# Kernel tuning notes

Hardware: AMD Instinct MI355X
Metric: run time of the kernel (lower is better)

## Reference

```python
import jax, jax.numpy as jnp
import numpy as np

B, T, C, H = 8, 2048, 768, 64

def setup_inputs() -> dict:
    key = jax.random.key(0)
    k1, k2, k3, k4 = jax.random.split(key, 4)
    x = jax.random.normal(k1, (B, T, C), dtype=jnp.float32)
    Wk = jax.random.normal(k2, (C, H), dtype=jnp.float32) * 0.02
    Wq = jax.random.normal(k3, (C, H), dtype=jnp.float32) * 0.02
    Wv = jax.random.normal(k4, (C, H), dtype=jnp.float32) * 0.02
    return {"x": x, "Wk": Wk, "Wq": Wq, "Wv": Wv}

def reference(x, Wk, Wq, Wv):
    # QKV projections (no bias): [B,T,C] @ [C,H] -> [B,T,H]
    k = jnp.einsum('btc,ch->bth', x, Wk)
    q = jnp.einsum('btc,ch->bth', x, Wq)
    v = jnp.einsum('btc,ch->bth', x, Wv)
    scale = 1.0 / jnp.sqrt(jnp.asarray(q.shape[-1], q.dtype))
    # scores: [B,T,T]
    wei = jnp.einsum('bth,bsh->bts', q, k) * scale
    # causal mask: upper triangle (k=1) set to -inf before softmax
    causal = jnp.tril(jnp.ones((wei.shape[1], wei.shape[2]), dtype=bool))
    wei = jnp.where(causal[None, :, :], wei, -jnp.inf)
    wei = jax.nn.softmax(wei, axis=-1)
    # dropout deterministic (training=False) -> identity
    out = jnp.einsum('bts,bsh->bth', wei, v)
    return out
```

## Files before the change

### kernel.cpp

```cpp
#include <hip/hip_runtime.h>
#include <hip/hip_bf16.h>
#include <stdint.h>

#define BB 8
#define TT 2048
#define CC 768
#define NTPB 72

typedef __bf16 bf16x8 __attribute__((ext_vector_type(8)));
typedef float f32x4 __attribute__((ext_vector_type(4)));
typedef float f32x16 __attribute__((ext_vector_type(16)));

__device__ inline __bf16 f2b(float f) {
    __hip_bfloat16 h = __float2bfloat16(f);
    return __builtin_bit_cast(__bf16, h);
}
__device__ inline ushort f2bits(float f) {
    __hip_bfloat16 h = __float2bfloat16(f);
    return __builtin_bit_cast(ushort, h);
}
__device__ inline float bits2f(ushort u) {
    return __builtin_bit_cast(float, ((uint32_t)u) << 16);
}
__device__ inline uint32_t cvtpk(float lo, float hi) {
    uint32_t r;
    asm("v_cvt_pk_bf16_f32 %0, %1, %2" : "=v"(r) : "v"(lo), "v"(hi));
    return r;
}
__device__ inline void pswap(uint32_t& a, uint32_t& b) {
    asm volatile("v_permlane32_swap_b32 %0, %1" : "+v"(a), "+v"(b));
}

#define GLL16(gp, lp)                                                          \
    __builtin_amdgcn_global_load_lds(                                          \
        (const __attribute__((address_space(1))) unsigned int*)(gp),           \
        (__attribute__((address_space(3))) unsigned int*)(lp), 16, 0, 0)

__launch_bounds__(256)
__global__ void wt_kernel(const float* __restrict__ Wk, const float* __restrict__ Wq,
                          const float* __restrict__ Wv, ushort* __restrict__ WtF) {
    __shared__ float tile[32][65];
    int m  = blockIdx.x / 24;
    int c0 = (blockIdx.x % 24) * 32;
    const float* W = (m == 0) ? Wq : ((m == 1) ? Wk : Wv);
    int tid = threadIdx.x;
    {
        int r   = tid >> 3;
        int col = (tid & 7) * 8;
        float4 v0 = *(const float4*)&W[(size_t)(c0 + r) * 64 + col];
        float4 v1 = *(const float4*)&W[(size_t)(c0 + r) * 64 + col + 4];
        tile[r][col]     = v0.x; tile[r][col + 1] = v0.y;
        tile[r][col + 2] = v0.z; tile[r][col + 3] = v0.w;
        tile[r][col + 4] = v1.x; tile[r][col + 5] = v1.y;
        tile[r][col + 6] = v1.z; tile[r][col + 7] = v1.w;
    }
    __syncthreads();
    int j   = tid >> 2;
    int sub = tid & 3;
    int cc  = sub * 8;
    ushort tmp[8];
#pragma unroll
    for (int e = 0; e < 8; e++) tmp[e] = f2bits(tile[cc + e][j]);
    int kc = c0 >> 5;
    ushort* dst = &WtF[((size_t)kc * 192 + m * 64 + j) * 32 + sub * 8];
    *(uint4*)(dst) = *(uint4*)&tmp[0];
}

__launch_bounds__(256, 3)
__global__ void qkv_kernel(const float* __restrict__ x, const ushort* __restrict__ WtF,
                           ushort* __restrict__ qws, ushort* __restrict__ kws,
                           ushort* __restrict__ vws) {
    __shared__ float  xsA[4][32 * 32];
    __shared__ ushort xsB[3][6144];

    int tid  = threadIdx.x;
    int wid  = tid >> 6;
    int lane = tid & 63;
    int l15  = lane & 15;
    int hi4  = lane >> 4;
    int row0 = blockIdx.x * 32;

    int rA  = tid >> 3;
    int gcA = (tid & 7) ^ (rA & 7);
    const float* gpA = x + (size_t)(row0 + rA) * CC + gcA * 4;

    int PB0 = tid, PB1 = tid + 256, PB2 = tid + 512;
    int LB0 = PB0 ^ ((PB0 >> 3) & 3);
    int LB1 = PB1 ^ ((PB1 >> 3) & 3);
    int LB2 = PB2 ^ ((PB2 >> 3) & 3);

    int PrB[3];
#pragma unroll
    for (int nt = 0; nt < 3; nt++) {
        int Lr = (wid * 48 + nt * 16 + l15) * 4 + hi4;
        PrB[nt] = Lr ^ ((Lr >> 3) & 3);
    }

    f32x4 acc[2][3];
#pragma unroll
    for (int mm = 0; mm < 2; mm++)
#pragma unroll
        for (int nt = 0; nt < 3; nt++) acc[mm][nt] = (f32x4){0.f, 0.f, 0.f, 0.f};

    auto stageA = [&](int t) {
        GLL16(gpA + t * 32, &xsA[t & 3][(size_t)tid * 4]);
    };
    auto stageB = [&](int t) {
        int buf = t % 3;
        const ushort* bsrc = WtF + (size_t)t * 6144;
        GLL16(bsrc + LB0 * 8, &xsB[buf][PB0 * 8]);
        GLL16(bsrc + LB1 * 8, &xsB[buf][PB1 * 8]);
        GLL16(bsrc + LB2 * 8, &xsB[buf][PB2 * 8]);
    };

    stageA(0); stageA(1);
    stageB(0); stageB(1);
    stageA(2); stageA(3);

#pragma unroll
    for (int p = 0; p < 12; p++) {
        if (p < 11) asm volatile("s_waitcnt vmcnt(2)" ::: "memory");
        else        asm volatile("s_waitcnt vmcnt(0)" ::: "memory");
        __builtin_amdgcn_s_barrier();
        __builtin_amdgcn_sched_barrier(0);

#pragma unroll
        for (int u = 0; u < 2; u++) {
            int t    = 2 * p + u;
            int bufA = t & 3;
            int bufB = t % 3;
            bf16x8 af[2];
#pragma unroll
            for (int mm = 0; mm < 2; mm++) {
                int row = mm * 16 + l15;
                const float* base = &xsA[bufA][row * 32];
                float4 fa = *(const float4*)(base + (((2 * hi4)     ^ (row & 7)) * 4));
                float4 fb = *(const float4*)(base + (((2 * hi4 + 1) ^ (row & 7)) * 4));
                uint32_t w0 = cvtpk(fa.x, fa.y), w1 = cvtpk(fa.z, fa.w);
                uint32_t w2 = cvtpk(fb.x, fb.y), w3 = cvtpk(fb.z, fb.w);
                uint4 u4 = {w0, w1, w2, w3};
                af[mm] = __builtin_bit_cast(bf16x8, u4);
            }
#pragma unroll
            for (int nt = 0; nt < 3; nt++) {
                bf16x8 b = __builtin_bit_cast(bf16x8, *(const uint4*)&xsB[bufB][PrB[nt] * 8]);
                acc[0][nt] = __builtin_amdgcn_mfma_f32_16x16x32_bf16(af[0], b, acc[0][nt], 0, 0, 0);
                acc[1][nt] = __builtin_amdgcn_mfma_f32_16x16x32_bf16(af[1], b, acc[1][nt], 0, 0, 0);
            }
        }
        __builtin_amdgcn_s_barrier();
        if (p < 11) { stageB(2 * p + 2); stageB(2 * p + 3); }
        if (p < 10) { stageA(2 * p + 4); stageA(2 * p + 5); }
    }

    const float qscale = 0.125f * 1.4426950408889634f;
    int bidx = row0 >> 11;
#pragma unroll
    for (int mm = 0; mm < 2; mm++) {
        int r0 = row0 + mm * 16 + 4 * hi4;
        int t0 = r0 & 2047;
#pragma unroll
        for (int nt = 0; nt < 3; nt++) {
            int c = wid * 48 + nt * 16 + l15;
            int m = c >> 6;
            int j = c & 63;
            if (m == 0) {
#pragma unroll
                for (int r = 0; r < 4; r++)
                    qws[(size_t)(r0 + r) * 64 + j] = f2bits(acc[mm][nt][r] * qscale);
            } else if (m == 1) {
#pragma unroll
                for (int r = 0; r < 4; r++)
                    kws[(size_t)(r0 + r) * 64 + j] = f2bits(acc[mm][nt][r]);
            } else {
                ushort4 pk;
                pk.x = f2bits(acc[mm][nt][0]);
                pk.y = f2bits(acc[mm][nt][1]);
                pk.z = f2bits(acc[mm][nt][2]);
                pk.w = f2bits(acc[mm][nt][3]);
                *(ushort4*)&vws[((size_t)bidx * 64 + j) * TT + t0] = pk;
            }
        }
    }
}

__launch_bounds__(256, 3)
__global__ void flash_kernel(const ushort* __restrict__ qg, const ushort* __restrict__ kg,
                             const ushort* __restrict__ vtg, float* __restrict__ out,
                             ushort* __restrict__ pO, float* __restrict__ pM,
                             float* __restrict__ pL) {
    __shared__ ushort Ks[3][64 * 64];
    __shared__ ushort Vs[3][64 * 64];

    int tid  = threadIdx.x;
    int wid  = tid >> 6;
    int lane = tid & 63;
    int l31  = lane & 31;
    int hi   = lane >> 5;

    int b  = blockIdx.x & 7;
    int tp = blockIdx.x >> 3;
    int g  = 0;
    while (tp >= ((g + 2) * (g + 2)) >> 2) g++;
    int seg   = tp - (((g + 1) * (g + 1)) >> 2);
    int nseg  = (g + 2) >> 1;
    int Qb    = g * 128;
    int Q0w   = Qb + wid * 32;
    int s_beg = seg * 256;
    int s_end = (s_beg + 256 < Qb + 128) ? s_beg + 256 : Qb + 128;
    int nt    = (s_end - s_beg) >> 6;

    int rS  = tid >> 3;
    int gcS = (tid & 7) ^ (rS & 7);
    const ushort* kS = kg  + ((size_t)b * TT + rS) * 64 + gcS * 8;
    const ushort* vS = vtg + ((size_t)b * 64 + rS) * TT + gcS * 8;

    auto stage = [&](int tt) {
        int buf = tt % 3;
        int ss  = s_beg + tt * 64;
        const ushort* kA = kS + (size_t)ss * 64;
        const ushort* vA = vS + ss;
        GLL16(kA,            &Ks[buf][tid * 8]);
        GLL16(kA + 32 * 64,  &Ks[buf][(tid + 256) * 8]);
        GLL16(vA,            &Vs[buf][tid * 8]);
        GLL16(vA + 32 * TT,  &Vs[buf][(tid + 256) * 8]);
    };

    const ushort* qp = qg + ((size_t)b * TT + Q0w + l31) * 64 + hi * 8;
    bf16x8 qf[4];
#pragma unroll
    for (int c = 0; c < 4; c++)
        qf[c] = __builtin_bit_cast(bf16x8, *(const uint4*)(qp + c * 16));

    f32x16 o0 = (f32x16)(0.f), o1 = (f32x16)(0.f);
    float m  = -INFINITY;
    float lp = 0.f;

    stage(0);
    if (nt > 1) stage(1);

    for (int t = 0; t < nt; t++) {
        if (t < nt - 1) asm volatile("s_waitcnt vmcnt(4)" ::: "memory");
        else            asm volatile("s_waitcnt vmcnt(0)" ::: "memory");
        __builtin_amdgcn_s_barrier();
        __builtin_amdgcn_sched_barrier(0);
        if (t + 2 < nt) stage(t + 2);

        int s0 = s_beg + t * 64;
        if (s0 < Q0w + 32) {
            int buf = t % 3;
            bf16x8 kf[2][4];
#pragma unroll
            for (int tt = 0; tt < 2; tt++) {
                int rk = tt * 32 + l31;
                const ushort* base = &Ks[buf][rk * 64];
                int sw = rk & 7;
#pragma unroll
                for (int c = 0; c < 4; c++)
                    kf[tt][c] = __builtin_bit_cast(bf16x8,
                        *(const uint4*)(base + (((c * 2 + hi) ^ sw) * 8)));
            }

            f32x16 st0 = (f32x16)(0.f), st1 = (f32x16)(0.f);
#pragma unroll
            for (int c = 0; c < 4; c++)
                st0 = __builtin_amdgcn_mfma_f32_32x32x16_bf16(kf[0][c], qf[c], st0, 0, 0, 0);
#pragma unroll
            for (int c = 0; c < 4; c++)
                st1 = __builtin_amdgcn_mfma_f32_32x32x16_bf16(kf[1][c], qf[c], st1, 0, 0, 0);

            if (s0 + 63 > Q0w) {
                int th0 = Q0w + l31 - s0 - 4 * hi;
                int th1 = th0 - 32;
#pragma unroll
                for (int r = 0; r < 16; r++) {
                    int kvl = (r & 3) + 8 * (r >> 2);
                    if (kvl > th0) st0[r] = -INFINITY;
                    if (kvl > th1) st1[r] = -INFINITY;
                }
            }

            float a[16];
#pragma unroll
            for (int r = 0; r < 16; r++) a[r] = fmaxf(st0[r], st1[r]);
#pragma unroll
            for (int off = 8; off > 0; off >>= 1)
#pragma unroll
                for (int i = 0; i < 8; i++)
                    if (i < off) a[i] = fmaxf(a[i], a[i + off]);
            float pmax = fmaxf(a[0], __shfl_xor(a[0], 32));
            if (__any(pmax > m + 11.54f)) {
                float mn = fmaxf(m, pmax);
                float al = exp2f(m - mn);
                lp *= al;
#pragma unroll
                for (int r = 0; r < 16; r++) { o0[r] *= al; o1[r] *= al; }
                m = mn;
            }
#pragma unroll
            for (int r = 0; r < 16; r++) {
                st0[r] = exp2f(st0[r] - m);
                st1[r] = exp2f(st1[r] - m);
            }
            float s[16];
#pragma unroll
            for (int r = 0; r < 16; r++) s[r] = st0[r] + st1[r];
#pragma unroll
            for (int off = 8; off > 0; off >>= 1)
#pragma unroll
                for (int i = 0; i < 8; i++)
                    if (i < off) s[i] += s[i + off];
            lp += s[0];

            bf16x8 pf[4];
            {
                uint32_t w0, w1, w2, w3;
                w0 = cvtpk(st0[0], st0[1]);  w1 = cvtpk(st0[2], st0[3]);
                w2 = cvtpk(st0[4], st0[5]);  w3 = cvtpk(st0[6], st0[7]);
                pswap(w0, w2); pswap(w1, w3);
                uint4 u0 = {w0, w1, w2, w3}; pf[0] = __builtin_bit_cast(bf16x8, u0);
                w0 = cvtpk(st0[8], st0[9]);  w1 = cvtpk(st0[10], st0[11]);
                w2 = cvtpk(st0[12], st0[13]); w3 = cvtpk(st0[14], st0[15]);
                pswap(w0, w2); pswap(w1, w3);
                uint4 u1 = {w0, w1, w2, w3}; pf[1] = __builtin_bit_cast(bf16x8, u1);
                w0 = cvtpk(st1[0], st1[1]);  w1 = cvtpk(st1[2], st1[3]);
                w2 = cvtpk(st1[4], st1[5]);  w3 = cvtpk(st1[6], st1[7]);
                pswap(w0, w2); pswap(w1, w3);
                uint4 u2 = {w0, w1, w2, w3}; pf[2] = __builtin_bit_cast(bf16x8, u2);
                w0 = cvtpk(st1[8], st1[9]);  w1 = cvtpk(st1[10], st1[11]);
                w2 = cvtpk(st1[12], st1[13]); w3 = cvtpk(st1[14], st1[15]);
                pswap(w0, w2); pswap(w1, w3);
                uint4 u3 = {w0, w1, w2, w3}; pf[3] = __builtin_bit_cast(bf16x8, u3);
            }

            bf16x8 vf[2][4];
#pragma unroll
            for (int ht = 0; ht < 2; ht++) {
                int rv = ht * 32 + l31;
                const ushort* base = &Vs[buf][rv * 64];
                int sw = rv & 7;
#pragma unroll
                for (int c = 0; c < 4; c++)
                    vf[ht][c] = __builtin_bit_cast(bf16x8,
                        *(const uint4*)(base + (((c * 2 + hi) ^ sw) * 8)));
            }

#pragma unroll
            for (int c = 0; c < 4; c++)
                o0 = __builtin_amdgcn_mfma_f32_32x32x16_bf16(vf[0][c], pf[c], o0, 0, 0, 0);
#pragma unroll
            for (int c = 0; c < 4; c++)
                o1 = __builtin_amdgcn_mfma_f32_32x32x16_bf16(vf[1][c], pf[c], o1, 0, 0, 0);
        }
    }

    float lsum = lp + __shfl_xor(lp, 32);

    if (nseg == 1) {
        float inv = 1.f / lsum;
        float* ob = out + ((size_t)b * TT + Q0w + l31) * 64;
#pragma unroll
        for (int gg = 0; gg < 4; gg++) {
            float4 v0 = {o0[4*gg] * inv, o0[4*gg+1] * inv, o0[4*gg+2] * inv, o0[4*gg+3] * inv};
            *(float4*)(ob + 8 * gg + 4 * hi) = v0;
            float4 v1 = {o1[4*gg] * inv, o1[4*gg+1] * inv, o1[4*gg+2] * inv, o1[4*gg+3] * inv};
            *(float4*)(ob + 32 + 8 * gg + 4 * hi) = v1;
        }
    } else {
        int tb = b * NTPB + tp;
        ushort* pb = pO + (size_t)tb * 8192 + (size_t)(wid * 32 + l31) * 64;
#pragma unroll
        for (int gg = 0; gg < 4; gg++) {
            ushort4 v0 = {f2bits(o0[4*gg]), f2bits(o0[4*gg+1]),
                          f2bits(o0[4*gg+2]), f2bits(o0[4*gg+3])};
            *(ushort4*)(pb + 8 * gg + 4 * hi) = v0;
            ushort4 v1 = {f2bits(o1[4*gg]), f2bits(o1[4*gg+1]),
                          f2bits(o1[4*gg+2]), f2bits(o1[4*gg+3])};
            *(ushort4*)(pb + 32 + 8 * gg + 4 * hi) = v1;
        }
        if (hi == 0) {
            pM[(size_t)tb * 128 + wid * 32 + l31] = m;
            pL[(size_t)tb * 128 + wid * 32 + l31] = lsum;
        }
    }
}

__launch_bounds__(256)
__global__ void merge_kernel(const ushort* __restrict__ pO, const float* __restrict__ pM,
                             const float* __restrict__ pL, float* __restrict__ out) {
    int b    = blockIdx.x / 56;
    int rem  = blockIdx.x % 56;
    int g    = 2 + (rem >> 2);
    int q4   = rem & 3;
    int nseg = (g + 2) >> 1;
    int tbase = b * NTPB + (((g + 1) * (g + 1)) >> 2);

    int row  = q4 * 32 + (threadIdx.x >> 3);
    int colg = (threadIdx.x & 7) * 8;

    float mstar = -INFINITY;
    for (int s = 0; s < nseg; s++)
        mstar = fmaxf(mstar, pM[(size_t)(tbase + s) * 128 + row]);

    float oa[8] = {0.f, 0.f, 0.f, 0.f, 0.f, 0.f, 0.f, 0.f};
    float la = 0.f;
    for (int s = 0; s < nseg; s++) {
        float w = exp2f(pM[(size_t)(tbase + s) * 128 + row] - mstar);
        la += w * pL[(size_t)(tbase + s) * 128 + row];
        uint4 u = *(const uint4*)&pO[(size_t)(tbase + s) * 8192 + (size_t)row * 64 + colg];
#pragma unroll
        for (int e = 0; e < 4; e++) {
            uint32_t wdw = ((const uint32_t*)&u)[e];
            oa[e*2]     += w * bits2f((ushort)(wdw & 0xffff));
            oa[e*2 + 1] += w * bits2f((ushort)(wdw >> 16));
        }
    }
    float inv = 1.f / la;
    float* ob = out + ((size_t)b * TT + g * 128 + row) * 64 + colg;
    float4 r0 = {oa[0] * inv, oa[1] * inv, oa[2] * inv, oa[3] * inv};
    float4 r1 = {oa[4] * inv, oa[5] * inv, oa[6] * inv, oa[7] * inv};
    *(float4*)(ob)     = r0;
    *(float4*)(ob + 4) = r1;
}

extern "C" void kernel_launch(void* const* d_in, const int* in_sizes, int n_in,
                              void* d_out, int out_size, void* d_ws, size_t ws_size,
                              hipStream_t stream) {
    const float* x  = (const float*)d_in[0];
    const float* Wk = (const float*)d_in[1];
    const float* Wq = (const float*)d_in[2];
    const float* Wv = (const float*)d_in[3];
    float* out = (float*)d_out;

    char* ws = (char*)d_ws;
    ushort* WtF = (ushort*)(ws);
    ushort* qws = (ushort*)(ws + 0x50000);
    ushort* kws = (ushort*)(ws + 0x250000);
    ushort* vws = (ushort*)(ws + 0x450000);
    ushort* pO  = (ushort*)(ws + 0x650000);
    float*  pM  = (float*)(ws + 0x1050000);
    float*  pL  = (float*)(ws + 0x1098000);

    wt_kernel<<<72, 256, 0, stream>>>(Wk, Wq, Wv, WtF);
    qkv_kernel<<<(BB * TT) / 32, 256, 0, stream>>>(x, WtF, qws, kws, vws);
    flash_kernel<<<BB * NTPB, 256, 0, stream>>>(qws, kws, vws, out, pO, pM, pL);
    merge_kernel<<<BB * 14 * 4, 256, 0, stream>>>(pO, pM, pL, out);
}
```

Baseline: 45.90 us.

## Enlarge flash query tile to 256 rows with 512-thread blocks

After: 49.27 us. 1.07x slower.

```diff
diff --git a/kernel.cpp b/kernel.cpp
--- a/kernel.cpp
+++ b/kernel.cpp
@@ -5,16 +5,12 @@
 #define BB 8
 #define TT 2048
 #define CC 768
-#define NTPB 72
+#define NTQB 36
 
 typedef __bf16 bf16x8 __attribute__((ext_vector_type(8)));
 typedef float f32x4 __attribute__((ext_vector_type(4)));
 typedef float f32x16 __attribute__((ext_vector_type(16)));
 
-__device__ inline __bf16 f2b(float f) {
-    __hip_bfloat16 h = __float2bfloat16(f);
-    return __builtin_bit_cast(__bf16, h);
-}
 __device__ inline ushort f2bits(float f) {
     __hip_bfloat16 h = __float2bfloat16(f);
     return __builtin_bit_cast(ushort, h);
@@ -184,8 +180,8 @@
     }
 }
 
-__launch_bounds__(256, 3)
-__global__ void flash_kernel(const ushort* __restrict__ qg, const ushort* __restrict__ kg,
+__launch_bounds__(512, 2)
+__global__ void flash_kernel(const ushort* __restrict__ qg_, const ushort* __restrict__ kg,
                              const ushort* __restrict__ vtg, float* __restrict__ out,
                              ushort* __restrict__ pO, float* __restrict__ pM,
                              float* __restrict__ pL) {
@@ -200,15 +196,13 @@
 
     int b  = blockIdx.x & 7;
     int tp = blockIdx.x >> 3;
-    int g  = 0;
-    while (tp >= ((g + 2) * (g + 2)) >> 2) g++;
-    int seg   = tp - (((g + 1) * (g + 1)) >> 2);
-    int nseg  = (g + 2) >> 1;
-    int Qb    = g * 128;
+    int qg = 0;
+    while (tp >= ((qg + 1) * (qg + 2)) >> 1) qg++;
+    int seg   = tp - ((qg * (qg + 1)) >> 1);
+    int nseg  = qg + 1;
+    int Qb    = qg * 256;
     int Q0w   = Qb + wid * 32;
     int s_beg = seg * 256;
-    int s_end = (s_beg + 256 < Qb + 128) ? s_beg + 256 : Qb + 128;
-    int nt    = (s_end - s_beg) >> 6;
 
     int rS  = tid >> 3;
     int gcS = (tid & 7) ^ (rS & 7);
@@ -218,15 +212,11 @@
     auto stage = [&](int tt) {
         int buf = tt % 3;
         int ss  = s_beg + tt * 64;
-        const ushort* kA = kS + (size_t)ss * 64;
-        const ushort* vA = vS + ss;
-        GLL16(kA,            &Ks[buf][tid * 8]);
-        GLL16(kA + 32 * 64,  &Ks[buf][(tid + 256) * 8]);
-        GLL16(vA,            &Vs[buf][tid * 8]);
-        GLL16(vA + 32 * TT,  &Vs[buf][(tid + 256) * 8]);
+        GLL16(kS + (size_t)ss * 64, &Ks[buf][tid * 8]);
+        GLL16(vS + ss,              &Vs[buf][tid * 8]);
     };
 
-    const ushort* qp = qg + ((size_t)b * TT + Q0w + l31) * 64 + hi * 8;
+    const ushort* qp = qg_ + ((size_t)b * TT + Q0w + l31) * 64 + hi * 8;
     bf16x8 qf[4];
 #pragma unroll
     for (int c = 0; c < 4; c++)
@@ -237,14 +227,15 @@
     float lp = 0.f;
 
     stage(0);
-    if (nt > 1) stage(1);
-
-    for (int t = 0; t < nt; t++) {
-        if (t < nt - 1) asm volatile("s_waitcnt vmcnt(4)" ::: "memory");
-        else            asm volatile("s_waitcnt vmcnt(0)" ::: "memory");
+    stage(1);
+
+#pragma unroll
+    for (int t = 0; t < 4; t++) {
+        if (t < 3) asm volatile("s_waitcnt vmcnt(2)" ::: "memory");
+        else       asm volatile("s_waitcnt vmcnt(0)" ::: "memory");
         __builtin_amdgcn_s_barrier();
         __builtin_amdgcn_sched_barrier(0);
-        if (t + 2 < nt) stage(t + 2);
+        if (t + 2 < 4) stage(t + 2);
 
         int s0 = s_beg + t * 64;
         if (s0 < Q0w + 32) {
@@ -367,8 +358,8 @@
             *(float4*)(ob + 32 + 8 * gg + 4 * hi) = v1;
         }
     } else {
-        int tb = b * NTPB + tp;
-        ushort* pb = pO + (size_t)tb * 8192 + (size_t)(wid * 32 + l31) * 64;
+        int tb = b * NTQB + tp;
+        ushort* pb = pO + (size_t)tb * 16384 + (size_t)(wid * 32 + l31) * 64;
 #pragma unroll
         for (int gg = 0; gg < 4; gg++) {
             ushort4 v0 = {f2bits(o0[4*gg]), f2bits(o0[4*gg+1]),
@@ -379,8 +370,8 @@
             *(ushort4*)(pb + 32 + 8 * gg + 4 * hi) = v1;
         }
         if (hi == 0) {
-            pM[(size_t)tb * 128 + wid * 32 + l31] = m;
-            pL[(size_t)tb * 128 + wid * 32 + l31] = lsum;
+            pM[(size_t)tb * 256 + wid * 32 + l31] = m;
+            pL[(size_t)tb * 256 + wid * 32 + l31] = lsum;
         }
     }
 }
@@ -388,26 +379,26 @@
 __launch_bounds__(256)
 __global__ void merge_kernel(const ushort* __restrict__ pO, const float* __restrict__ pM,
                              const float* __restrict__ pL, float* __restrict__ out) {
-    int b    = blockIdx.x / 56;
-    int rem  = blockIdx.x % 56;
-    int g    = 2 + (rem >> 2);
-    int q4   = rem & 3;
-    int nseg = (g + 2) >> 1;
-    int tbase = b * NTPB + (((g + 1) * (g + 1)) >> 2);
-
-    int row  = q4 * 32 + (threadIdx.x >> 3);
+    int b    = blockIdx.x & 7;
+    int rem  = blockIdx.x >> 3;
+    int qg   = 1 + (rem >> 3);
+    int q8   = rem & 7;
+    int nseg = qg + 1;
+    int tbase = b * NTQB + ((qg * (qg + 1)) >> 1);
+
+    int row  = q8 * 32 + (threadIdx.x >> 3);
     int colg = (threadIdx.x & 7) * 8;
 
     float mstar = -INFINITY;
     for (int s = 0; s < nseg; s++)
-        mstar = fmaxf(mstar, pM[(size_t)(tbase + s) * 128 + row]);
+        mstar = fmaxf(mstar, pM[(size_t)(tbase + s) * 256 + row]);
 
     float oa[8] = {0.f, 0.f, 0.f, 0.f, 0.f, 0.f, 0.f, 0.f};
     float la = 0.f;
     for (int s = 0; s < nseg; s++) {
-        float w = exp2f(pM[(size_t)(tbase + s) * 128 + row] - mstar);
-        la += w * pL[(size_t)(tbase + s) * 128 + row];
-        uint4 u = *(const uint4*)&pO[(size_t)(tbase + s) * 8192 + (size_t)row * 64 + colg];
+        float w = exp2f(pM[(size_t)(tbase + s) * 256 + row] - mstar);
+        la += w * pL[(size_t)(tbase + s) * 256 + row];
+        uint4 u = *(const uint4*)&pO[(size_t)(tbase + s) * 16384 + (size_t)row * 64 + colg];
 #pragma unroll
         for (int e = 0; e < 4; e++) {
             uint32_t wdw = ((const uint32_t*)&u)[e];
@@ -416,7 +407,7 @@
         }
     }
     float inv = 1.f / la;
-    float* ob = out + ((size_t)b * TT + g * 128 + row) * 64 + colg;
+    float* ob = out + ((size_t)b * TT + qg * 256 + row) * 64 + colg;
     float4 r0 = {oa[0] * inv, oa[1] * inv, oa[2] * inv, oa[3] * inv};
     float4 r1 = {oa[4] * inv, oa[5] * inv, oa[6] * inv, oa[7] * inv};
     *(float4*)(ob)     = r0;
@@ -443,6 +434,6 @@
 
     wt_kernel<<<72, 256, 0, stream>>>(Wk, Wq, Wv, WtF);
     qkv_kernel<<<(BB * TT) / 32, 256, 0, stream>>>(x, WtF, qws, kws, vws);
-    flash_kernel<<<BB * NTPB, 256, 0, stream>>>(qws, kws, vws, out, pO, pM, pL);
-    merge_kernel<<<BB * 14 * 4, 256, 0, stream>>>(pO, pM, pL, out);
-}
+    flash_kernel<<<BB * NTQB, 512, 0, stream>>>(qws, kws, vws, out, pO, pM, pL);
+    merge_kernel<<<8 * 7 * 8, 256, 0, stream>>>(pO, pM, pL, out);
+}
```
